# Kernel tuning notes

Measured on AMD Instinct MI355X. Metric: run time of the kernel, lower is better.

Reference implementation:

```python
import jax, jax.numpy as jnp
import numpy as np

S, N, C = 16384, 2048, 8  # n_samples, n_channels, n_components

def setup_inputs() -> dict:
    key = jax.random.key(0)
    k1, k2, k3, k4 = jax.random.split(key, 4)
    return {
        "inputs": jax.random.uniform(k1, (S, N), dtype=jnp.float32),
        "components": jax.random.uniform(k2, (C, N), dtype=jnp.float32),
        "contributions": jax.random.uniform(k3, (S, C), dtype=jnp.float32),
        "shift": jax.random.normal(k4, (S, C), dtype=jnp.float32) * 3.0,
    }

def reference(inputs, components, contributions, shift):
    # fit_shift=True branch. The original builds k_matrix[i,j] = j - i and
    # coeff[i,j] = clip(1 - |shift - (j - i)|, 0, 1), then dots with the
    # component. That is exactly linear interpolation of component at
    # position i + shift, with zero padding outside [0, N-1].
    n_samples, n_channels = inputs.shape
    n_comp = components.shape[0]
    i = jnp.arange(n_channels, dtype=shift.dtype)
    pos = i[None, None, :] + shift[:, :, None]            # [S, C, N]
    j0f = jnp.floor(pos)
    frac = pos - j0f                                      # in [0, 1)
    j0 = j0f.astype(jnp.int32)
    j1 = j0 + 1
    cidx = jnp.arange(n_comp)[None, :, None]              # broadcast over [S, C, N]
    g0 = components[cidx, jnp.clip(j0, 0, n_channels - 1)]
    g1 = components[cidx, jnp.clip(j1, 0, n_channels - 1)]
    v0 = ((j0 >= 0) & (j0 < n_channels)).astype(components.dtype)
    v1 = ((j1 >= 0) & (j1 < n_channels)).astype(components.dtype)
    shifted = g0 * (1.0 - frac) * v0 + g1 * frac * v1     # [S, C, N] shifted components
    # scale by per-sample contributions and sum over components
    return jnp.einsum('scn,sc->sn', shifted, contributions)
```

## Files before the change

kernel.cpp:

```cpp
#include <hip/hip_runtime.h>
#include <hip/hip_fp16.h>


namespace {
constexpr int kS = 16384;
constexpr int kN = 2048;
constexpr int kC = 8;
constexpr int kK = 320;
constexpr int kSlots = 40;
constexpr size_t kGtBytes = (size_t)kN * kK * 2;
constexpr size_t kABytes  = (size_t)kS * kK * 2;
constexpr size_t kWsNeed  = kGtBytes + kABytes;

typedef _Float16 f16x8 __attribute__((ext_vector_type(8)));
typedef float    f32x4 __attribute__((ext_vector_type(4)));

__global__ __launch_bounds__(256)
void zeroA_kernel(uint4* __restrict__ a4) {
    const int idx = blockIdx.x * 256 + threadIdx.x;
    const int n4  = (int)(kABytes / 16);
    if (idx < n4) a4[idx] = make_uint4(0u, 0u, 0u, 0u);
}

__global__ __launch_bounds__(256)
void buildG_kernel(const float* __restrict__ comps, __half* __restrict__ Gt) {
    const int tid = blockIdx.x * 256 + threadIdx.x;
    const int c = tid >> 11;
    const int n = tid & 2047;
    const float* src = comps + c * kN;

    uint32_t w[kSlots / 2];
    #pragma unroll
    for (int t2 = 0; t2 < kSlots / 2; ++t2) {
        uint32_t pk = 0;
        #pragma unroll
        for (int h = 0; h < 2; ++h) {
            const int t = 2 * t2 + h;
            float v = 0.f;
            if (t < 35) {
                const int j = n + (t - 17);
                if (j >= 0 && j < kN) v = src[j];
            }
            const __half hv = __float2half_rn(v);
            pk |= (uint32_t)__half_as_ushort(hv) << (16 * h);
        }
        w[t2] = pk;
    }
    uint4* dst = reinterpret_cast<uint4*>(Gt + (size_t)n * kK + c * kSlots);
    #pragma unroll
    for (int i = 0; i < kSlots / 8; ++i)
        dst[i] = make_uint4(w[4 * i], w[4 * i + 1], w[4 * i + 2], w[4 * i + 3]);
}

__global__ __launch_bounds__(256)
void buildA_kernel(const float* __restrict__ contrib,
                   const float* __restrict__ shift,
                   __half* __restrict__ A) {
    const int tid = blockIdx.x * 256 + threadIdx.x;
    const int s = tid >> 3;
    const int c = tid & 7;
    const float ctv = contrib[(size_t)s * kC + c];
    const float sv  = shift[(size_t)s * kC + c];
    float fl = floorf(sv);
    int d = (int)fl;
    d = d < -17 ? -17 : (d > 16 ? 16 : d);
    const float fr = sv - (float)d;
    const __half w1h = __float2half_rn(ctv * fr);
    const __half w0h = __float2half_rn(ctv - __half2float(w1h));
    __half* row = A + (size_t)s * kK + c * kSlots;
    row[d + 17] = w0h;
    row[d + 18] = w1h;
}

__global__ __launch_bounds__(256, 2)
void gemm_kernel(const __half* __restrict__ A, const __half* __restrict__ Gt,
                 float* __restrict__ out) {
    __shared__ __align__(16) __half At[128 * 64];
    __shared__ __align__(16) __half Bt[128 * 64];

    const int tid = threadIdx.x;
    const int bm = blockIdx.x >> 4;
    const int bn = blockIdx.x & 15;
    const int s0 = bm * 128, n0 = bn * 128;

    const int rbase = tid >> 3;
    const int t8    = tid & 7;
    const __half* srcA[4];
    const __half* srcB[4];
    int dst[4];
    #pragma unroll
    for (int q = 0; q < 4; ++q) {
        const int rr = q * 32 + rbase;
        const int slot = t8 ^ (rr & 7);
        srcA[q] = A  + (size_t)(s0 + rr) * kK + slot * 8;
        srcB[q] = Gt + (size_t)(n0 + rr) * kK + slot * 8;
        dst[q]  = rr * 64 + t8 * 8;
    }

    const int lane = tid & 63, wave = tid >> 6;
    const int wm = (wave >> 1) * 64, wn = (wave & 1) * 64;
    const int l15 = lane & 15, l4 = lane >> 4, p = lane & 7;
    const int aOff0 = (wm + l15) * 64 + ((l4)     ^ p) * 8;
    const int aOff1 = (wm + l15) * 64 + ((4 + l4) ^ p) * 8;
    const int bOff0 = (wn + l15) * 64 + ((l4)     ^ p) * 8;
    const int bOff1 = (wn + l15) * 64 + ((4 + l4) ^ p) * 8;

    f32x4 acc[4][4];
    #pragma unroll
    for (int mi = 0; mi < 4; ++mi)
        #pragma unroll
        for (int ni = 0; ni < 4; ++ni)
            acc[mi][ni] = f32x4{0.f, 0.f, 0.f, 0.f};

    uint4 ta[4], tb[4];
    #pragma unroll
    for (int q = 0; q < 4; ++q) {
        ta[q] = *reinterpret_cast<const uint4*>(srcA[q]);
        tb[q] = *reinterpret_cast<const uint4*>(srcB[q]);
    }

    #pragma unroll 1
    for (int step = 0; step < 5; ++step) {
        #pragma unroll
        for (int q = 0; q < 4; ++q) {
            *reinterpret_cast<uint4*>(&At[dst[q]]) = ta[q];
            *reinterpret_cast<uint4*>(&Bt[dst[q]]) = tb[q];
        }
        __syncthreads();
        if (step < 4) {
            #pragma unroll
            for (int q = 0; q < 4; ++q) {
                srcA[q] += 64; srcB[q] += 64;
                ta[q] = *reinterpret_cast<const uint4*>(srcA[q]);
                tb[q] = *reinterpret_cast<const uint4*>(srcB[q]);
            }
        }
        #pragma unroll
        for (int ks = 0; ks < 2; ++ks) {
            const int ao = ks ? aOff1 : aOff0;
            const int bo = ks ? bOff1 : bOff0;
            f16x8 af[4], bf[4];
            #pragma unroll
            for (int mi = 0; mi < 4; ++mi)
                af[mi] = *reinterpret_cast<const f16x8*>(&At[ao + mi * 1024]);
            #pragma unroll
            for (int ni = 0; ni < 4; ++ni)
                bf[ni] = *reinterpret_cast<const f16x8*>(&Bt[bo + ni * 1024]);
            #pragma unroll
            for (int mi = 0; mi < 4; ++mi)
                #pragma unroll
                for (int ni = 0; ni < 4; ++ni)
                    acc[mi][ni] = __builtin_amdgcn_mfma_f32_16x16x32_f16(
                        af[mi], bf[ni], acc[mi][ni], 0, 0, 0);
        }
        __syncthreads();
    }

    #pragma unroll
    for (int mi = 0; mi < 4; ++mi) {
        #pragma unroll
        for (int v = 0; v < 4; ++v) {
            float* orow = out + (size_t)(s0 + wm + mi * 16 + l4 * 4 + v) * kN
                              + n0 + wn + l15;
            #pragma unroll
            for (int ni = 0; ni < 4; ++ni) orow[ni * 16] = acc[mi][ni][v];
        }
    }
}

constexpr int kMf     = 16;
constexpr int kBlockF = 512;
constexpr int kPadH  = 32;
constexpr int kUnits = 1057;
constexpr int kRowStride = 1192;
__device__ __forceinline__ int swz(int u) { return u + (u >> 3); }

__global__ __launch_bounds__(kBlockF, 8)
void smf_kernel(const float* __restrict__ comps,
                const float* __restrict__ contrib,
                const float* __restrict__ shift,
                float* __restrict__ out)
{
    __shared__ uint32_t ldsU[kC * kRowStride];
    __shared__ float    ctLds[kMf * kC];
    __shared__ float    shLds[kMf * kC];

    const int tid = threadIdx.x;
    const int s0  = blockIdx.x * kMf;

    for (int c = 0; c < kC; ++c) {
        const float* src = comps + c * kN;
        uint32_t* dstp = ldsU + c * kRowStride;
        for (int u = tid; u < kUnits; u += kBlockF) {
            const int j = 2 * u - kPadH;
            float2 v = make_float2(0.f, 0.f);
            if (j >= 0 && j < kN - 1) v = *reinterpret_cast<const float2*>(src + j);
            __half2 h2 = __floats2half2_rn(v.x, v.y);
            dstp[swz(u)] = *reinterpret_cast<const uint32_t*>(&h2);
        }
    }
    for (int tt = tid; tt < (kMf * kC) / 2; tt += kBlockF) {
        if (tt < (kMf * kC) / 4) {
            reinterpret_cast<float4*>(ctLds)[tt] =
                reinterpret_cast<const float4*>(contrib + (size_t)s0 * kC)[tt];
        } else {
            const int t2 = tt - (kMf * kC) / 4;
            reinterpret_cast<float4*>(shLds)[t2] =
                reinterpret_cast<const float4*>(shift + (size_t)s0 * kC)[t2];
        }
    }
    __syncthreads();

    const int q = tid >> 8;
    const int t = tid & 255;

    #pragma unroll 1
    for (int r = 0; r < kMf / 2; ++r) {
        const int si = q * (kMf / 2) + r;
        const int s  = s0 + si;
        const float4 ccA = *reinterpret_cast<const float4*>(ctLds + si * kC);
        const float4 ccB = *reinterpret_cast<const float4*>(ctLds + si * kC + 4);
        const float4 csA = *reinterpret_cast<const float4*>(shLds + si * kC);
        const float4 csB = *reinterpret_cast<const float4*>(shLds + si * kC + 4);
        const float ct[8] = {ccA.x, ccA.y, ccA.z, ccA.w, ccB.x, ccB.y, ccB.z, ccB.w};
        const float sh[8] = {csA.x, csA.y, csA.z, csA.w, csB.x, csB.y, csB.z, csB.w};
        float accA[4], accB[4];
        #pragma unroll
        for (int k = 0; k < 4; ++k) { accA[k] = 0.f; accB[k] = 0.f; }
        #pragma unroll
        for (int c = 0; c < kC; ++c) {
            const float fl = floorf(sh[c]);
            const float fr = sh[c] - fl;
            int d = (int)fl;
            d = d < -31 ? -31 : (d > 31 ? 31 : d);
            const float w1 = ct[c] * fr;
            const float w0 = ct[c] - w1;
            const int a   = 4 * t + d + kPadH;
            const int u0  = a >> 1;
            const bool odd = (a & 1) != 0;
            const uint32_t* row = ldsU + c * kRowStride;
            const uint32_t yA0 = row[swz(u0 + 0)];
            const uint32_t yA1 = row[swz(u0 + 1)];
            const uint32_t yA2 = row[swz(u0 + 2)];
            const uint32_t yB0 = row[swz(u0 + 512)];
            const uint32_t yB1 = row[swz(u0 + 513)];
            const uint32_t yB2 = row[swz(u0 + 514)];
            const uint32_t zA0 = odd ? __builtin_amdgcn_alignbit(yA1, yA0, 16) : yA0;
            const uint32_t zA1 = odd ? __builtin_amdgcn_alignbit(yA2, yA1, 16) : yA1;
            const uint32_t zA2 = odd ? (yA2 >> 16) : yA2;
            const uint32_t zB0 = odd ? __builtin_amdgcn_alignbit(yB1, yB0, 16) : yB0;
            const uint32_t zB1 = odd ? __builtin_amdgcn_alignbit(yB2, yB1, 16) : yB1;
            const uint32_t zB2 = odd ? (yB2 >> 16) : yB2;
            const float2 fA0 = __half22float2(*reinterpret_cast<const __half2*>(&zA0));
            const float2 fA1 = __half22float2(*reinterpret_cast<const __half2*>(&zA1));
            const float2 fA2 = __half22float2(*reinterpret_cast<const __half2*>(&zA2));
            const float2 fB0 = __half22float2(*reinterpret_cast<const __half2*>(&zB0));
            const float2 fB1 = __half22float2(*reinterpret_cast<const __half2*>(&zB1));
            const float2 fB2 = __half22float2(*reinterpret_cast<const __half2*>(&zB2));
            accA[0] += w0 * fA0.x + w1 * fA0.y;
            accA[1] += w0 * fA0.y + w1 * fA1.x;
            accA[2] += w0 * fA1.x + w1 * fA1.y;
            accA[3] += w0 * fA1.y + w1 * fA2.x;
            accB[0] += w0 * fB0.x + w1 * fB0.y;
            accB[1] += w0 * fB0.y + w1 * fB1.x;
            accB[2] += w0 * fB1.x + w1 * fB1.y;
            accB[3] += w0 * fB1.y + w1 * fB2.x;
        }
        float* orow = out + (size_t)s * kN;
        *reinterpret_cast<float4*>(orow + 4 * t) =
            make_float4(accA[0], accA[1], accA[2], accA[3]);
        *reinterpret_cast<float4*>(orow + 1024 + 4 * t) =
            make_float4(accB[0], accB[1], accB[2], accB[3]);
    }
}
}

extern "C" void kernel_launch(void* const* d_in, const int* in_sizes, int n_in,
                              void* d_out, int out_size, void* d_ws, size_t ws_size,
                              hipStream_t stream) {
    const float* comps   = (const float*)d_in[1];
    const float* contrib = (const float*)d_in[2];
    const float* shiftp  = (const float*)d_in[3];
    float* out = (float*)d_out;

    if (ws_size >= kWsNeed && d_ws != nullptr) {
        __half* Gt = (__half*)d_ws;
        __half* A  = (__half*)((char*)d_ws + kGtBytes);
        zeroA_kernel<<<dim3((int)(kABytes / 16 / 256)), dim3(256), 0, stream>>>(
            (uint4*)A);
        buildG_kernel<<<dim3((kC * kN) / 256), dim3(256), 0, stream>>>(comps, Gt);
        buildA_kernel<<<dim3((kS * kC) / 256), dim3(256), 0, stream>>>(contrib, shiftp, A);
        gemm_kernel<<<dim3((kS / 128) * (kN / 128)), dim3(256), 0, stream>>>(A, Gt, out);
    } else {
        smf_kernel<<<dim3(kS / kMf), dim3(kBlockF), 0, stream>>>(comps, contrib, shiftp, out);
    }
}
```

Baseline: 320.7 us.

## Fuse sparse A-matrix construction into GEMM and keep full-K A tile resident

Drops the separate zero-fill and A-build kernels along with the 10 MB fp16 A matrix in workspace. Each 512-thread block now builds its 64-row A tile directly in LDS from contrib and shift, keeps all K=320 A fragments in registers, and sweeps over the 16 column tiles of G. Output is staged through LDS so it can be written as coalesced nontemporal float4 stores. This removes the launches and global traffic tied to A. In exchange, LDS use per block is much larger (about 158 KB), which limits occupancy, and register pressure rises from holding af[10][2].

After: 294.2 us. 1.09x faster.

```diff
diff --git a/kernel.cpp b/kernel.cpp
--- a/kernel.cpp
+++ b/kernel.cpp
@@ -9,18 +9,10 @@
 constexpr int kK = 320;
 constexpr int kSlots = 40;
 constexpr size_t kGtBytes = (size_t)kN * kK * 2;
-constexpr size_t kABytes  = (size_t)kS * kK * 2;
-constexpr size_t kWsNeed  = kGtBytes + kABytes;
+constexpr size_t kWsNeed  = kGtBytes;
 
 typedef _Float16 f16x8 __attribute__((ext_vector_type(8)));
 typedef float    f32x4 __attribute__((ext_vector_type(4)));
-
-__global__ __launch_bounds__(256)
-void zeroA_kernel(uint4* __restrict__ a4) {
-    const int idx = blockIdx.x * 256 + threadIdx.x;
-    const int n4  = (int)(kABytes / 16);
-    if (idx < n4) a4[idx] = make_uint4(0u, 0u, 0u, 0u);
-}
 
 __global__ __launch_bounds__(256)
 void buildG_kernel(const float* __restrict__ comps, __half* __restrict__ Gt) {
@@ -52,118 +44,128 @@
         dst[i] = make_uint4(w[4 * i], w[4 * i + 1], w[4 * i + 2], w[4 * i + 3]);
 }
 
-__global__ __launch_bounds__(256)
-void buildA_kernel(const float* __restrict__ contrib,
-                   const float* __restrict__ shift,
-                   __half* __restrict__ A) {
-    const int tid = blockIdx.x * 256 + threadIdx.x;
-    const int s = tid >> 3;
-    const int c = tid & 7;
-    const float ctv = contrib[(size_t)s * kC + c];
-    const float sv  = shift[(size_t)s * kC + c];
-    float fl = floorf(sv);
-    int d = (int)fl;
-    d = d < -17 ? -17 : (d > 16 ? 16 : d);
-    const float fr = sv - (float)d;
-    const __half w1h = __float2half_rn(ctv * fr);
-    const __half w0h = __float2half_rn(ctv - __half2float(w1h));
-    __half* row = A + (size_t)s * kK + c * kSlots;
-    row[d + 17] = w0h;
-    row[d + 18] = w1h;
-}
-
-__global__ __launch_bounds__(256, 2)
-void gemm_kernel(const __half* __restrict__ A, const __half* __restrict__ Gt,
-                 float* __restrict__ out) {
-    __shared__ __align__(16) __half At[128 * 64];
-    __shared__ __align__(16) __half Bt[128 * 64];
+__global__ __launch_bounds__(512, 2)
+void gemm_kernel(const float* __restrict__ contrib,
+                 const float* __restrict__ shift,
+                 const __half* __restrict__ Gt,
+                 float* __restrict__ out)
+{
+    __shared__ __half Atile[64 * kK];
+    __shared__ __half Btile[128 * kK];
+    __shared__ float  outB[64 * 136];
 
     const int tid = threadIdx.x;
-    const int bm = blockIdx.x >> 4;
-    const int bn = blockIdx.x & 15;
-    const int s0 = bm * 128, n0 = bn * 128;
-
-    const int rbase = tid >> 3;
-    const int t8    = tid & 7;
-    const __half* srcA[4];
-    const __half* srcB[4];
-    int dst[4];
-    #pragma unroll
-    for (int q = 0; q < 4; ++q) {
-        const int rr = q * 32 + rbase;
-        const int slot = t8 ^ (rr & 7);
-        srcA[q] = A  + (size_t)(s0 + rr) * kK + slot * 8;
-        srcB[q] = Gt + (size_t)(n0 + rr) * kK + slot * 8;
-        dst[q]  = rr * 64 + t8 * 8;
-    }
-
-    const int lane = tid & 63, wave = tid >> 6;
-    const int wm = (wave >> 1) * 64, wn = (wave & 1) * 64;
-    const int l15 = lane & 15, l4 = lane >> 4, p = lane & 7;
-    const int aOff0 = (wm + l15) * 64 + ((l4)     ^ p) * 8;
-    const int aOff1 = (wm + l15) * 64 + ((4 + l4) ^ p) * 8;
-    const int bOff0 = (wn + l15) * 64 + ((l4)     ^ p) * 8;
-    const int bOff1 = (wn + l15) * 64 + ((4 + l4) ^ p) * 8;
-
-    f32x4 acc[4][4];
-    #pragma unroll
-    for (int mi = 0; mi < 4; ++mi)
-        #pragma unroll
-        for (int ni = 0; ni < 4; ++ni)
-            acc[mi][ni] = f32x4{0.f, 0.f, 0.f, 0.f};
-
-    uint4 ta[4], tb[4];
-    #pragma unroll
-    for (int q = 0; q < 4; ++q) {
-        ta[q] = *reinterpret_cast<const uint4*>(srcA[q]);
-        tb[q] = *reinterpret_cast<const uint4*>(srcB[q]);
-    }
+    const int s0  = blockIdx.x * 64;
+
+    const int rr = tid >> 2;
+    const int sb = tid & 3;
+    const int xw = rr & 7;
+    uint4 tb[10];
+    {
+        const __half* g = Gt + (size_t)rr * kK;
+        #pragma unroll
+        for (int q = 0; q < 10; ++q)
+            tb[q] = *reinterpret_cast<const uint4*>(g + (sb + 4 * q) * 8);
+    }
+
+    #pragma unroll
+    for (int i = 0; i < 5; ++i)
+        reinterpret_cast<uint4*>(Atile)[i * 512 + tid] = make_uint4(0u,0u,0u,0u);
+    __syncthreads();
+    {
+        const int sr = tid >> 3;
+        const int c  = tid & 7;
+        const float ctv = contrib[(size_t)(s0 + sr) * kC + c];
+        const float sv  = shift[(size_t)(s0 + sr) * kC + c];
+        int d = (int)floorf(sv);
+        d = d < -17 ? -17 : (d > 16 ? 16 : d);
+        const float fr = sv - (float)d;
+        const __half w1h = __float2half_rn(ctv * fr);
+        const __half w0h = __float2half_rn(ctv - __half2float(w1h));
+        const int h0 = c * kSlots + d + 17;
+        const int h1 = h0 + 1;
+        const int x  = sr & 7;
+        Atile[sr * kK + (((h0 >> 3) ^ x) << 3) + (h0 & 7)] = w0h;
+        Atile[sr * kK + (((h1 >> 3) ^ x) << 3) + (h1 & 7)] = w1h;
+    }
+    __syncthreads();
+
+    const int lane = tid & 63;
+    const int wave = tid >> 6;
+    const int wm = (wave >> 2) * 32;
+    const int wn = (wave & 3) * 32;
+    const int l15 = lane & 15, l4 = lane >> 4;
+
+    f16x8 af[10][2];
+    #pragma unroll
+    for (int mi = 0; mi < 2; ++mi) {
+        const int r = wm + mi * 16 + l15;
+        const int x = r & 7;
+        #pragma unroll
+        for (int ks = 0; ks < 10; ++ks) {
+            const int sl = (ks * 4 + l4) ^ x;
+            af[ks][mi] = *reinterpret_cast<const f16x8*>(&Atile[r * kK + sl * 8]);
+        }
+    }
+
+    const int rB0 = wn + l15, rB1 = rB0 + 16;
+    const int xB0 = rB0 & 7,  xB1 = rB1 & 7;
+    const int bBase0 = rB0 * kK, bBase1 = rB1 * kK;
 
     #pragma unroll 1
-    for (int step = 0; step < 5; ++step) {
-        #pragma unroll
-        for (int q = 0; q < 4; ++q) {
-            *reinterpret_cast<uint4*>(&At[dst[q]]) = ta[q];
-            *reinterpret_cast<uint4*>(&Bt[dst[q]]) = tb[q];
-        }
+    for (int step = 0; step < 16; ++step) {
         __syncthreads();
-        if (step < 4) {
+
+        {
+            __half* drow = Btile + rr * kK;
             #pragma unroll
-            for (int q = 0; q < 4; ++q) {
-                srcA[q] += 64; srcB[q] += 64;
-                ta[q] = *reinterpret_cast<const uint4*>(srcA[q]);
-                tb[q] = *reinterpret_cast<const uint4*>(srcB[q]);
+            for (int q = 0; q < 10; ++q) {
+                const int sl = (sb + 4 * q) ^ xw;
+                *reinterpret_cast<uint4*>(drow + sl * 8) = tb[q];
             }
         }
-        #pragma unroll
-        for (int ks = 0; ks < 2; ++ks) {
-            const int ao = ks ? aOff1 : aOff0;
-            const int bo = ks ? bOff1 : bOff0;
-            f16x8 af[4], bf[4];
+        __syncthreads();
+
+        if (step < 15) {
+            const __half* g = Gt + ((size_t)(step + 1) * 128 + rr) * kK;
             #pragma unroll
-            for (int mi = 0; mi < 4; ++mi)
-                af[mi] = *reinterpret_cast<const f16x8*>(&At[ao + mi * 1024]);
-            #pragma unroll
-            for (int ni = 0; ni < 4; ++ni)
-                bf[ni] = *reinterpret_cast<const f16x8*>(&Bt[bo + ni * 1024]);
-            #pragma unroll
-            for (int mi = 0; mi < 4; ++mi)
-                #pragma unroll
-                for (int ni = 0; ni < 4; ++ni)
-                    acc[mi][ni] = __builtin_amdgcn_mfma_f32_16x16x32_f16(
-                        af[mi], bf[ni], acc[mi][ni], 0, 0, 0);
+            for (int q = 0; q < 10; ++q)
+                tb[q] = *reinterpret_cast<const uint4*>(g + (sb + 4 * q) * 8);
+        }
+
+        f32x4 acc00 = {0.f,0.f,0.f,0.f}, acc01 = {0.f,0.f,0.f,0.f};
+        f32x4 acc10 = {0.f,0.f,0.f,0.f}, acc11 = {0.f,0.f,0.f,0.f};
+        #pragma unroll
+        for (int ks = 0; ks < 10; ++ks) {
+            const int kq = ks * 4 + l4;
+            const f16x8 b0 = *reinterpret_cast<const f16x8*>(
+                &Btile[bBase0 + ((kq ^ xB0) << 3)]);
+            const f16x8 b1 = *reinterpret_cast<const f16x8*>(
+                &Btile[bBase1 + ((kq ^ xB1) << 3)]);
+            acc00 = __builtin_amdgcn_mfma_f32_16x16x32_f16(af[ks][0], b0, acc00, 0,0,0);
+            acc01 = __builtin_amdgcn_mfma_f32_16x16x32_f16(af[ks][0], b1, acc01, 0,0,0);
+            acc10 = __builtin_amdgcn_mfma_f32_16x16x32_f16(af[ks][1], b0, acc10, 0,0,0);
+            acc11 = __builtin_amdgcn_mfma_f32_16x16x32_f16(af[ks][1], b1, acc11, 0,0,0);
+        }
+
+        #pragma unroll
+        for (int v = 0; v < 4; ++v) {
+            outB[(wm +  0 + l4*4 + v) * 136 + wn +  0 + l15] = acc00[v];
+            outB[(wm +  0 + l4*4 + v) * 136 + wn + 16 + l15] = acc01[v];
+            outB[(wm + 16 + l4*4 + v) * 136 + wn +  0 + l15] = acc10[v];
+            outB[(wm + 16 + l4*4 + v) * 136 + wn + 16 + l15] = acc11[v];
         }
         __syncthreads();
-    }
-
-    #pragma unroll
-    for (int mi = 0; mi < 4; ++mi) {
-        #pragma unroll
-        for (int v = 0; v < 4; ++v) {
-            float* orow = out + (size_t)(s0 + wm + mi * 16 + l4 * 4 + v) * kN
-                              + n0 + wn + l15;
-            #pragma unroll
-            for (int ni = 0; ni < 4; ++ni) orow[ni * 16] = acc[mi][ni][v];
+
+        const int n0 = step * 128;
+        #pragma unroll
+        for (int k2 = 0; k2 < 4; ++k2) {
+            const int f   = k2 * 512 + tid;
+            const int row = f >> 5;
+            const int c4  = f & 31;
+            const f32x4 val = *reinterpret_cast<const f32x4*>(&outB[row * 136 + c4 * 4]);
+            __builtin_nontemporal_store(val,
+                reinterpret_cast<f32x4*>(out + (size_t)(s0 + row) * kN + n0 + c4 * 4));
         }
     }
 }
@@ -285,12 +287,8 @@
 
     if (ws_size >= kWsNeed && d_ws != nullptr) {
         __half* Gt = (__half*)d_ws;
-        __half* A  = (__half*)((char*)d_ws + kGtBytes);
-        zeroA_kernel<<<dim3((int)(kABytes / 16 / 256)), dim3(256), 0, stream>>>(
-            (uint4*)A);
         buildG_kernel<<<dim3((kC * kN) / 256), dim3(256), 0, stream>>>(comps, Gt);
-        buildA_kernel<<<dim3((kS * kC) / 256), dim3(256), 0, stream>>>(contrib, shiftp, A);
-        gemm_kernel<<<dim3((kS / 128) * (kN / 128)), dim3(256), 0, stream>>>(A, Gt, out);
+        gemm_kernel<<<dim3(kS / 64), dim3(512), 0, stream>>>(contrib, shiftp, Gt, out);
     } else {
         smf_kernel<<<dim3(kS / kMf), dim3(kBlockF), 0, stream>>>(comps, contrib, shiftp, out);
     }
```
